# Kernel optimization log

Measured on AMD Instinct MI355X. Metric: run time of the kernel, lower is better.

## Reference

```python
import jax, jax.numpy as jnp
import numpy as np


def setup_inputs() -> dict:
    key = jax.random.key(0)
    ks = jax.random.split(key, 5)
    B, S, I, H, O = 64, 2048, 128, 512, 128
    inputs = jax.random.normal(ks[0], (B, S, I), dtype=jnp.float32)
    h0 = jnp.zeros((B, H), dtype=jnp.float32)
    # Xavier-uniform for W_in / W_out, orthogonal-ish scaled for W_rec
    lim_in = float(np.sqrt(6.0 / (I + H)))
    W_in_w = jax.random.uniform(ks[1], (H, I), minval=-lim_in, maxval=lim_in, dtype=jnp.float32)
    W_in_b = jnp.zeros((H,), dtype=jnp.float32)
    # orthogonal init scaled by 0.9 (matches nn.init.orthogonal_ * 0.9)
    A = jax.random.normal(ks[2], (H, H), dtype=jnp.float32)
    Q, _ = jnp.linalg.qr(A)
    W_rec_w = (0.9 * Q).astype(jnp.float32)
    lim_out = float(np.sqrt(6.0 / (H + O)))
    W_out_w = jax.random.uniform(ks[3], (O, H), minval=-lim_out, maxval=lim_out, dtype=jnp.float32)
    W_out_b = jnp.zeros((O,), dtype=jnp.float32)
    return {
        "inputs": inputs, "h0": h0,
        "W_in_w": W_in_w, "W_in_b": W_in_b,
        "W_rec_w": W_rec_w,
        "W_out_w": W_out_w, "W_out_b": W_out_b,
    }


def reference(inputs, h0, W_in_w, W_in_b, W_rec_w, W_out_w, W_out_b):
    # Precompute the input projection for all timesteps in one big GEMM:
    # (B, S, I) @ (I, H) -> (B, S, H). Faithful: W_in(x_t) = x_t @ W_in_w.T + b.
    xin = jnp.einsum('bsi,hi->bsh', inputs, W_in_w) + W_in_b

    def step(h, x_t):  # x_t: (B, H) pre-projected input at time t
        h_new = jnp.tanh(x_t + h @ W_rec_w.T)  # W_rec has no bias
        return h_new, h_new

    # scan over time axis; move time to leading axis
    h_final, hs = jax.lax.scan(step, h0, jnp.swapaxes(xin, 0, 1))  # hs: (S, B, H)
    hs = jnp.swapaxes(hs, 0, 1)  # (B, S, H)
    outputs = jnp.einsum('bsh,oh->bso', hs, W_out_w) + W_out_b  # (B, S, O)
    return outputs, h_final
```

## Files before the change

### kernel.cpp

```cpp
#include <hip/hip_runtime.h>


typedef _Float16 half2_t __attribute__((ext_vector_type(2)));
typedef _Float16 half8_t __attribute__((ext_vector_type(8)));
typedef float    float2_t __attribute__((ext_vector_type(2)));
typedef float    float4_t __attribute__((ext_vector_type(4)));

#define BB 64
#define SS 2048
#define IN 128
#define HH 512
#define OO 128

using u16 = unsigned short;
using u32 = unsigned int;
using u64 = unsigned long long;

__device__ __forceinline__ float fdot2f(half2_t a, half2_t b, float c) {
#if __has_builtin(__builtin_amdgcn_fdot2)
    return __builtin_amdgcn_fdot2(a, b, c, false);
#else
    return c + (float)a[0] * (float)b[0] + (float)a[1] * (float)b[1];
#endif
}
__device__ __forceinline__ half2_t h2(float a, float b) {
    return half2_t{(_Float16)a, (_Float16)b};
}
__device__ __forceinline__ float fast_tanh(float x) {
    x = fminf(8.0f, fmaxf(-8.0f, x));
#if __has_builtin(__builtin_amdgcn_exp2f) && __has_builtin(__builtin_amdgcn_rcpf)
    const float t = __builtin_amdgcn_exp2f(x * 2.885390081777927f);
    return 1.0f - 2.0f * __builtin_amdgcn_rcpf(t + 1.0f);
#else
    return tanhf(x);
#endif
}
__device__ __forceinline__ void barrier_lds() {
    asm volatile("s_waitcnt lgkmcnt(0)\n\ts_barrier" ::: "memory");
}

__device__ __forceinline__ float red8(float v) {
    int i;
    i = __builtin_amdgcn_update_dpp(0, __builtin_bit_cast(int, v),
                                    0xB1, 0xF, 0xF, true);
    v += __builtin_bit_cast(float, i);
    i = __builtin_amdgcn_update_dpp(0, __builtin_bit_cast(int, v),
                                    0x4E, 0xF, 0xF, true);
    v += __builtin_bit_cast(float, i);
    i = __builtin_amdgcn_update_dpp(0, __builtin_bit_cast(int, v),
                                    0x141, 0xF, 0xF, true);
    v += __builtin_bit_cast(float, i);
    return v;
}
__device__ __forceinline__ float sel8(const float a[8], int c) {
    float v = a[0];
    v = (c == 1) ? a[1] : v;  v = (c == 2) ? a[2] : v;
    v = (c == 3) ? a[3] : v;  v = (c == 4) ? a[4] : v;
    v = (c == 5) ? a[5] : v;  v = (c == 6) ? a[6] : v;
    v = (c == 7) ? a[7] : v;
    return v;
}

__global__ __launch_bounds__(512, 2) void rnn_xin(
    const float* __restrict__ inputs,
    const float* __restrict__ W_in,
    const float* __restrict__ W_in_b,
    u16* __restrict__ xws)
{
    const int tid = threadIdx.x;
    const int c   = tid & 7;
    const int q   = tid >> 3;
    const float bmy = W_in_b[tid];

    half2_t wi8[8][8];
    #pragma unroll
    for (int jj = 0; jj < 8; ++jj) {
        const float4_t* r = (const float4_t*)(W_in + (q * 8 + jj) * IN + c * 16);
        #pragma unroll
        for (int m = 0; m < 4; ++m) {
            const float4_t u = r[m];
            wi8[jj][m * 2 + 0] = h2(u[0], u[1]);
            wi8[jj][m * 2 + 1] = h2(u[2], u[3]);
        }
    }

    const int row0 = blockIdx.x * 512;
    for (int r = 0; r < 512; ++r) {
        const size_t row = row0 + r;
        const float4_t* xr = (const float4_t*)(inputs + row * IN + c * 16);
        half2_t xv[8];
        #pragma unroll
        for (int m = 0; m < 4; ++m) {
            const float4_t u = xr[m];
            xv[m * 2 + 0] = h2(u[0], u[1]);
            xv[m * 2 + 1] = h2(u[2], u[3]);
        }
        float acc[8] = {0, 0, 0, 0, 0, 0, 0, 0};
        #pragma unroll
        for (int jj = 0; jj < 8; ++jj)
            #pragma unroll
            for (int m = 0; m < 8; ++m)
                acc[jj] = fdot2f(wi8[jj][m], xv[m], acc[jj]);
        #pragma unroll
        for (int jj = 0; jj < 8; ++jj) acc[jj] = red8(acc[jj]);
        const float out = sel8(acc, c) + bmy;
        const _Float16 hf = (_Float16)out;
        xws[row * HH + tid] = __builtin_bit_cast(u16, hf);
    }
}

#define REC_STEP(RB, WB, T)                                                  \
    do {                                                                     \
        u16 xn = 0;                                                          \
        if ((T) + 1 < SS) xn = xp[(size_t)((T) + 1) * HH + tid];             \
        float acc[8] = {0, 0, 0, 0, 0, 0, 0, 0};                             \
        const half2_t* hb = &(RB)[c * 36];                                   \
        _Pragma("unroll")                                                    \
        for (int kb = 0; kb < 8; ++kb) {                                     \
            const half8_t hv = *(const half8_t*)(hb + kb * 4);               \
            const half2_t p0 = __builtin_shufflevector(hv, hv, 0, 1);        \
            const half2_t p1 = __builtin_shufflevector(hv, hv, 2, 3);        \
            const half2_t p2 = __builtin_shufflevector(hv, hv, 4, 5);        \
            const half2_t p3 = __builtin_shufflevector(hv, hv, 6, 7);        \
            _Pragma("unroll")                                                \
            for (int jj = 0; jj < 6; ++jj) {                                 \
                acc[jj] = fdot2f(wr[jj][kb * 4 + 0], p0, acc[jj]);           \
                acc[jj] = fdot2f(wr[jj][kb * 4 + 1], p1, acc[jj]);           \
                acc[jj] = fdot2f(wr[jj][kb * 4 + 2], p2, acc[jj]);           \
                acc[jj] = fdot2f(wr[jj][kb * 4 + 3], p3, acc[jj]);           \
            }                                                                \
            const half8_t w6 = *(const half8_t*)(wb6 + (size_t)kb * 2048);   \
            acc[6] = fdot2f(__builtin_shufflevector(w6, w6, 0, 1), p0, acc[6]); \
            acc[6] = fdot2f(__builtin_shufflevector(w6, w6, 2, 3), p1, acc[6]); \
            acc[6] = fdot2f(__builtin_shufflevector(w6, w6, 4, 5), p2, acc[6]); \
            acc[6] = fdot2f(__builtin_shufflevector(w6, w6, 6, 7), p3, acc[6]); \
            const half8_t w7 = *(const half8_t*)(wb7 + (size_t)kb * 2048);   \
            acc[7] = fdot2f(__builtin_shufflevector(w7, w7, 0, 1), p0, acc[7]); \
            acc[7] = fdot2f(__builtin_shufflevector(w7, w7, 2, 3), p1, acc[7]); \
            acc[7] = fdot2f(__builtin_shufflevector(w7, w7, 4, 5), p2, acc[7]); \
            acc[7] = fdot2f(__builtin_shufflevector(w7, w7, 6, 7), p3, acc[7]); \
        }                                                                    \
        _Pragma("unroll")                                                    \
        for (int jj = 0; jj < 8; ++jj) acc[jj] = red8(acc[jj]);              \
        const float hv_new = fast_tanh(sel8(acc, c) + (float)xr);            \
        const _Float16 hf = (_Float16)hv_new;                                \
        xp[(size_t)(T) * HH + tid] = __builtin_bit_cast(u16, hf);            \
        ((_Float16*)(WB))[(tid >> 6) * 72 + (tid & 63)] = hf;                \
        if ((T) == SS - 1) hfinal[bb * HH + tid] = hv_new;                   \
        xr = __builtin_bit_cast(_Float16, xn);                               \
        barrier_lds();                                                       \
    } while (0)

__global__ __launch_bounds__(512, 2) void rnn_rec(
    const float* __restrict__ h0,
    const float* __restrict__ W_rec,
    u16* __restrict__ xws,
    float* __restrict__ hfinal)
{
    const int tid = threadIdx.x;
    const int bb  = blockIdx.x;
    const int c   = tid & 7;
    const int q   = tid >> 3;

    __shared__ __align__(16) half2_t wlin[2 * 8 * 512 * 4];
    __shared__ __align__(16) half2_t hbuf[2][288];

    half2_t wr[6][32];
    #pragma unroll
    for (int jj = 0; jj < 6; ++jj) {
        const float4_t* r = (const float4_t*)(W_rec + (q * 8 + jj) * HH + c * 64);
        #pragma unroll
        for (int m = 0; m < 16; ++m) {
            const float4_t u = r[m];
            wr[jj][m * 2 + 0] = h2(u[0], u[1]);
            wr[jj][m * 2 + 1] = h2(u[2], u[3]);
        }
    }
    #pragma unroll
    for (int jl = 0; jl < 2; ++jl) {
        const int j = q * 8 + 6 + jl;
        #pragma unroll
        for (int kb = 0; kb < 8; ++kb) {
            const float4_t u0 = *(const float4_t*)(W_rec + j * HH + c * 64 + kb * 8);
            const float4_t u1 = *(const float4_t*)(W_rec + j * HH + c * 64 + kb * 8 + 4);
            half8_t pack = half8_t{
                (_Float16)u0[0], (_Float16)u0[1], (_Float16)u0[2], (_Float16)u0[3],
                (_Float16)u1[0], (_Float16)u1[1], (_Float16)u1[2], (_Float16)u1[3]};
            *(half8_t*)&wlin[((jl * 8 + kb) * 512 + tid) * 4] = pack;
        }
    }
    ((_Float16*)hbuf[0])[(tid >> 6) * 72 + (tid & 63)] = (_Float16)h0[bb * HH + tid];

    u16* xp = xws + (size_t)bb * SS * HH;
    _Float16 xr = __builtin_bit_cast(_Float16, xp[tid]);
    __syncthreads();

    const half2_t* wb6 = &wlin[(size_t)tid * 4];
    const half2_t* wb7 = &wlin[(size_t)(8 * 512 + tid) * 4];

    for (int t = 0; t < SS; t += 2) {
        REC_STEP(hbuf[0], hbuf[1], t);
        REC_STEP(hbuf[1], hbuf[0], t + 1);
    }
}

__global__ __launch_bounds__(512, 2) void rnn_out(
    const u16* __restrict__ xws,
    const float* __restrict__ W_out,
    const float* __restrict__ W_out_b,
    float* __restrict__ outp)
{
    const int tid = threadIdx.x;
    const int c   = tid & 7;
    const int wv  = tid >> 6;
    const int lq  = (tid >> 3) & 7;
    const int o0  = wv * 16 + lq * 2;

    half2_t wo2[2][32];
    #pragma unroll
    for (int oo = 0; oo < 2; ++oo) {
        const float4_t* r = (const float4_t*)(W_out + (o0 + oo) * HH + c * 64);
        #pragma unroll
        for (int m = 0; m < 16; ++m) {
            const float4_t u = r[m];
            wo2[oo][m * 2 + 0] = h2(u[0], u[1]);
            wo2[oo][m * 2 + 1] = h2(u[2], u[3]);
        }
    }
    const float b0 = W_out_b[o0], b1 = W_out_b[o0 + 1];

    const int row0 = blockIdx.x * 512;
    for (int r = 0; r < 512; ++r) {
        const size_t row = row0 + r;
        const _Float16* hsrow = (const _Float16*)xws + row * HH + c * 64;
        float a0 = 0.f, a1 = 0.f;
        #pragma unroll
        for (int kb = 0; kb < 8; ++kb) {
            const half8_t hv = *(const half8_t*)(hsrow + kb * 8);
            const half2_t p0 = __builtin_shufflevector(hv, hv, 0, 1);
            const half2_t p1 = __builtin_shufflevector(hv, hv, 2, 3);
            const half2_t p2 = __builtin_shufflevector(hv, hv, 4, 5);
            const half2_t p3 = __builtin_shufflevector(hv, hv, 6, 7);
            a0 = fdot2f(wo2[0][kb * 4 + 0], p0, a0);
            a0 = fdot2f(wo2[0][kb * 4 + 1], p1, a0);
            a0 = fdot2f(wo2[0][kb * 4 + 2], p2, a0);
            a0 = fdot2f(wo2[0][kb * 4 + 3], p3, a0);
            a1 = fdot2f(wo2[1][kb * 4 + 0], p0, a1);
            a1 = fdot2f(wo2[1][kb * 4 + 1], p1, a1);
            a1 = fdot2f(wo2[1][kb * 4 + 2], p2, a1);
            a1 = fdot2f(wo2[1][kb * 4 + 3], p3, a1);
        }
        a0 = red8(a0);
        a1 = red8(a1);
        if (c == 0)
            *(float2_t*)(outp + row * OO + o0) = float2_t{a0 + b0, a1 + b1};
    }
}

__global__ __launch_bounds__(512, 1) void rnn_fused_fb(
    const float* __restrict__ inputs, const float* __restrict__ h0,
    const float* __restrict__ W_in, const float* __restrict__ W_in_b,
    const float* __restrict__ W_rec, const float* __restrict__ W_out,
    const float* __restrict__ W_out_b, float* __restrict__ outp,
    float* __restrict__ hfinal, u64* __restrict__ hex)
{
    const int tid = threadIdx.x;
    const int bb = blockIdx.x >> 1;
    const int w  = blockIdx.x & 1;
    const int c  = tid & 7;
    const int q  = tid >> 3;
    const int og = w * 64 + q;
    const int s  = c >> 2;
    const int oc = w * 4 + (c & 3);
    const int pc = (1 - w) * 4 + (c & 3);
    const int pw = 1 - w;

    __shared__ __align__(16) half2_t hbuf[288];
    __shared__ __align__(16) half2_t xh[2][96];

    half2_t wro[4][16]; half2_t wrp[4][16]; half2_t wi[4][8];
    half2_t woo[16]; half2_t wop[16]; float bias[4];

    #pragma unroll
    for (int jj = 0; jj < 4; ++jj) {
        const int jg = w * 256 + q * 4 + jj;
        const float4_t* ro = (const float4_t*)(W_rec + jg * HH + oc * 64 + s * 32);
        const float4_t* rp = (const float4_t*)(W_rec + jg * HH + pc * 64 + s * 32);
        #pragma unroll
        for (int m = 0; m < 8; ++m) {
            const float4_t uo = ro[m];
            wro[jj][m * 2 + 0] = h2(uo[0], uo[1]);
            wro[jj][m * 2 + 1] = h2(uo[2], uo[3]);
            const float4_t up = rp[m];
            wrp[jj][m * 2 + 0] = h2(up[0], up[1]);
            wrp[jj][m * 2 + 1] = h2(up[2], up[3]);
        }
        const float4_t* irow = (const float4_t*)(W_in + jg * IN + c * 16);
        #pragma unroll
        for (int m = 0; m < 4; ++m) {
            const float4_t u = irow[m];
            wi[jj][m * 2 + 0] = h2(u[0], u[1]);
            wi[jj][m * 2 + 1] = h2(u[2], u[3]);
        }
        bias[jj] = W_in_b[jg];
    }
    {
        const float4_t* oo = (const float4_t*)(W_out + og * HH + oc * 64 + s * 32);
        const float4_t* op = (const float4_t*)(W_out + og * HH + pc * 64 + s * 32);
        #pragma unroll
        for (int m = 0; m < 8; ++m) {
            const float4_t uo = oo[m];
            woo[m * 2 + 0] = h2(uo[0], uo[1]);
            woo[m * 2 + 1] = h2(uo[2], uo[3]);
            const float4_t up = op[m];
            wop[m * 2 + 0] = h2(up[0], up[1]);
            wop[m * 2 + 1] = h2(up[2], up[3]);
        }
    }
    const float bo = W_out_b[og];

    if (tid < 256) {
        const float2_t u = *(const float2_t*)(h0 + bb * HH + tid * 2);
        const int k = tid * 2;
        hbuf[(k >> 6) * 36 + ((k & 63) >> 1)] = h2(u[0], u[1]);
    }
    if (tid >= 256 && tid < 320) {
        const int i2 = tid - 256;
        const float2_t u = *(const float2_t*)(inputs + (size_t)(bb * SS) * IN + i2 * 2);
        xh[0][(i2 >> 3) * 12 + (i2 & 7)] = h2(u[0], u[1]);
    }
    __syncthreads();

    for (int t = 0; t < SS; ++t) {
        const int cur = t & 1;
        float2_t xr;
        const bool xload = (tid >= 256 && tid < 320) && (t + 1 < SS);
        if (xload)
            xr = *(const float2_t*)(inputs + (size_t)(bb * SS + (t + 1)) * IN + (tid - 256) * 2);

        float acc[4] = {0.f, 0.f, 0.f, 0.f};
        float oa = 0.f;
        {
            const half2_t* hb = &hbuf[oc * 36 + s * 16];
            #pragma unroll
            for (int ob = 0; ob < 4; ++ob) {
                const half8_t hv = *(const half8_t*)(hb + ob * 4);
                const half2_t p0 = __builtin_shufflevector(hv, hv, 0, 1);
                const half2_t p1 = __builtin_shufflevector(hv, hv, 2, 3);
                const half2_t p2 = __builtin_shufflevector(hv, hv, 4, 5);
                const half2_t p3 = __builtin_shufflevector(hv, hv, 6, 7);
                #pragma unroll
                for (int jj = 0; jj < 4; ++jj) {
                    acc[jj] = fdot2f(wro[jj][ob * 4 + 0], p0, acc[jj]);
                    acc[jj] = fdot2f(wro[jj][ob * 4 + 1], p1, acc[jj]);
                    acc[jj] = fdot2f(wro[jj][ob * 4 + 2], p2, acc[jj]);
                    acc[jj] = fdot2f(wro[jj][ob * 4 + 3], p3, acc[jj]);
                }
                oa = fdot2f(woo[ob * 4 + 0], p0, oa);
                oa = fdot2f(woo[ob * 4 + 1], p1, oa);
                oa = fdot2f(woo[ob * 4 + 2], p2, oa);
                oa = fdot2f(woo[ob * 4 + 3], p3, oa);
            }
        }
        const int sidx = ((bb * 2 + pw) * 2 + (cur ^ 1)) * 128 + tid;
        u64 spec = 0;
        if (t > 0 && tid < 128)
            spec = __hip_atomic_load(&hex[sidx], __ATOMIC_RELAXED,
                                     __HIP_MEMORY_SCOPE_AGENT);
        {
            const half2_t* xb = &xh[cur][c * 12];
            const half8_t xv0 = *(const half8_t*)(xb);
            const half8_t xv1 = *(const half8_t*)(xb + 4);
            const half2_t x0 = __builtin_shufflevector(xv0, xv0, 0, 1);
            const half2_t x1 = __builtin_shufflevector(xv0, xv0, 2, 3);
            const half2_t x2 = __builtin_shufflevector(xv0, xv0, 4, 5);
            const half2_t x3 = __builtin_shufflevector(xv0, xv0, 6, 7);
            const half2_t x4 = __builtin_shufflevector(xv1, xv1, 0, 1);
            const half2_t x5 = __builtin_shufflevector(xv1, xv1, 2, 3);
            const half2_t x6 = __builtin_shufflevector(xv1, xv1, 4, 5);
            const half2_t x7 = __builtin_shufflevector(xv1, xv1, 6, 7);
            #pragma unroll
            for (int jj = 0; jj < 4; ++jj) {
                acc[jj] = fdot2f(wi[jj][0], x0, acc[jj]);
                acc[jj] = fdot2f(wi[jj][1], x1, acc[jj]);
                acc[jj] = fdot2f(wi[jj][2], x2, acc[jj]);
                acc[jj] = fdot2f(wi[jj][3], x3, acc[jj]);
                acc[jj] = fdot2f(wi[jj][4], x4, acc[jj]);
                acc[jj] = fdot2f(wi[jj][5], x5, acc[jj]);
                acc[jj] = fdot2f(wi[jj][6], x6, acc[jj]);
                acc[jj] = fdot2f(wi[jj][7], x7, acc[jj]);
            }
        }
        if (t > 0 && tid < 128) {
            u64 v = spec;
            if ((u32)(v >> 32) != (u32)t) {
                do {
                    v = __hip_atomic_load(&hex[sidx], __ATOMIC_RELAXED,
                                          __HIP_MEMORY_SCOPE_AGENT);
                } while ((u32)(v >> 32) != (u32)t);
            }
            const int kg = pw * 256 + tid * 2;
            hbuf[(kg >> 6) * 36 + ((kg & 63) >> 1)] =
                __builtin_bit_cast(half2_t, (u32)v);
        }
        barrier_lds();
        {
            const half2_t* hb = &hbuf[pc * 36 + s * 16];
            #pragma unroll
            for (int ob = 0; ob < 4; ++ob) {
                const half8_t hv = *(const half8_t*)(hb + ob * 4);
                const half2_t p0 = __builtin_shufflevector(hv, hv, 0, 1);
                const half2_t p1 = __builtin_shufflevector(hv, hv, 2, 3);
                const half2_t p2 = __builtin_shufflevector(hv, hv, 4, 5);
                const half2_t p3 = __builtin_shufflevector(hv, hv, 6, 7);
                #pragma unroll
                for (int jj = 0; jj < 4; ++jj) {
                    acc[jj] = fdot2f(wrp[jj][ob * 4 + 0], p0, acc[jj]);
                    acc[jj] = fdot2f(wrp[jj][ob * 4 + 1], p1, acc[jj]);
                    acc[jj] = fdot2f(wrp[jj][ob * 4 + 2], p2, acc[jj]);
                    acc[jj] = fdot2f(wrp[jj][ob * 4 + 3], p3, acc[jj]);
                }
                oa = fdot2f(wop[ob * 4 + 0], p0, oa);
                oa = fdot2f(wop[ob * 4 + 1], p1, oa);
                oa = fdot2f(wop[ob * 4 + 2], p2, oa);
                oa = fdot2f(wop[ob * 4 + 3], p3, oa);
            }
        }
        #pragma unroll
        for (int jj = 0; jj < 4; ++jj) {
            float v = acc[jj];
            v += __shfl_xor(v, 1);
            v += __shfl_xor(v, 2);
            v += __shfl_xor(v, 4);
            acc[jj] = v;
        }
        oa += __shfl_xor(oa, 1);
        oa += __shfl_xor(oa, 2);
        oa += __shfl_xor(oa, 4);
        {
            const bool hi = (c & 1) != 0;
            const float a0 = hi ? acc[2] : acc[0];
            const float a1 = hi ? acc[3] : acc[1];
            const float b0 = hi ? bias[2] : bias[0];
            const float b1 = hi ? bias[3] : bias[1];
            const float va = fast_tanh(a0 + b0);
            const float vb = fast_tanh(a1 + b1);
            if (c < 2) {
                const half2_t hx = h2(va, vb);
                const u64 pay = (((u64)(u32)(t + 1)) << 32) |
                                (u64)__builtin_bit_cast(u32, hx);
                const int slot = ((bb * 2 + w) * 2 + cur) * 128 + q * 2 + c;
                __hip_atomic_store(&hex[slot], pay, __ATOMIC_RELAXED,
                                   __HIP_MEMORY_SCOPE_AGENT);
                const int kg = w * 256 + q * 4 + c * 2;
                hbuf[(kg >> 6) * 36 + ((kg & 63) >> 1)] = hx;
                if (t == SS - 1)
                    *(float2_t*)(&hfinal[bb * HH + w * 256 + q * 4 + c * 2]) =
                        float2_t{va, vb};
            }
            if (c == 2 && t > 0)
                outp[(size_t)(bb * SS + (t - 1)) * OO + og] = oa + bo;
        }
        if (xload) {
            const int i2 = tid - 256;
            xh[cur ^ 1][(i2 >> 3) * 12 + (i2 & 7)] = h2(xr[0], xr[1]);
        }
        barrier_lds();
    }

    if (tid < 128) {
        const int sidx = ((bb * 2 + pw) * 2 + ((SS - 1) & 1)) * 128 + tid;
        u64 v;
        do {
            v = __hip_atomic_load(&hex[sidx], __ATOMIC_RELAXED,
                                  __HIP_MEMORY_SCOPE_AGENT);
        } while ((u32)(v >> 32) != (u32)SS);
        const int kg = pw * 256 + tid * 2;
        hbuf[(kg >> 6) * 36 + ((kg & 63) >> 1)] =
            __builtin_bit_cast(half2_t, (u32)v);
    }
    __syncthreads();
    {
        float oa = 0.f;
        const half2_t* ho = &hbuf[oc * 36 + s * 16];
        const half2_t* hp = &hbuf[pc * 36 + s * 16];
        #pragma unroll
        for (int ob = 0; ob < 4; ++ob) {
            const half8_t hv = *(const half8_t*)(ho + ob * 4);
            oa = fdot2f(woo[ob * 4 + 0], __builtin_shufflevector(hv, hv, 0, 1), oa);
            oa = fdot2f(woo[ob * 4 + 1], __builtin_shufflevector(hv, hv, 2, 3), oa);
            oa = fdot2f(woo[ob * 4 + 2], __builtin_shufflevector(hv, hv, 4, 5), oa);
            oa = fdot2f(woo[ob * 4 + 3], __builtin_shufflevector(hv, hv, 6, 7), oa);
        }
        #pragma unroll
        for (int ob = 0; ob < 4; ++ob) {
            const half8_t hv = *(const half8_t*)(hp + ob * 4);
            oa = fdot2f(wop[ob * 4 + 0], __builtin_shufflevector(hv, hv, 0, 1), oa);
            oa = fdot2f(wop[ob * 4 + 1], __builtin_shufflevector(hv, hv, 2, 3), oa);
            oa = fdot2f(wop[ob * 4 + 2], __builtin_shufflevector(hv, hv, 4, 5), oa);
            oa = fdot2f(wop[ob * 4 + 3], __builtin_shufflevector(hv, hv, 6, 7), oa);
        }
        oa += __shfl_xor(oa, 1);
        oa += __shfl_xor(oa, 2);
        oa += __shfl_xor(oa, 4);
        if (c == 0)
            outp[(size_t)(bb * SS + (SS - 1)) * OO + og] = oa + bo;
    }
}

extern "C" void kernel_launch(void* const* d_in, const int* in_sizes, int n_in,
                              void* d_out, int out_size, void* d_ws, size_t ws_size,
                              hipStream_t stream) {
    const float* inputs  = (const float*)d_in[0];
    const float* h0      = (const float*)d_in[1];
    const float* W_in_w  = (const float*)d_in[2];
    const float* W_in_b  = (const float*)d_in[3];
    const float* W_rec_w = (const float*)d_in[4];
    const float* W_out_w = (const float*)d_in[5];
    const float* W_out_b = (const float*)d_in[6];

    float* out    = (float*)d_out;
    float* hfinal = out + (size_t)BB * SS * OO;

    const size_t xin_bytes = (size_t)BB * SS * HH * sizeof(u16);
    if (ws_size >= xin_bytes) {
        u16* xws = (u16*)d_ws;
        rnn_xin<<<dim3(256), dim3(512), 0, stream>>>(inputs, W_in_w, W_in_b, xws);
        rnn_rec<<<dim3(BB), dim3(512), 0, stream>>>(h0, W_rec_w, xws, hfinal);
        rnn_out<<<dim3(256), dim3(512), 0, stream>>>(xws, W_out_w, W_out_b, out);
    } else {
        u64* hex = (u64*)d_ws;
        rnn_fused_fb<<<dim3(BB * 2), dim3(512), 0, stream>>>(
            inputs, h0, W_in_w, W_in_b, W_rec_w, W_out_w, W_out_b,
            out, hfinal, hex);
    }
}
```

Measured before the change: 4.462 ms.

## Keep seven recurrent weight rows in registers, double-buffer input loads, split GEMM grids

```diff
diff --git a/kernel.cpp b/kernel.cpp
--- a/kernel.cpp
+++ b/kernel.cpp
@@ -61,6 +61,32 @@
     return v;
 }
 
+#define XLOAD(B, R)                                                          \
+    do {                                                                     \
+        const float4_t* xr_ = (const float4_t*)(inputs + (size_t)(R) * IN + c * 16); \
+        (B)[0] = xr_[0]; (B)[1] = xr_[1]; (B)[2] = xr_[2]; (B)[3] = xr_[3];  \
+    } while (0)
+#define XCOMP(B, R)                                                          \
+    do {                                                                     \
+        half2_t xv[8];                                                       \
+        _Pragma("unroll")                                                    \
+        for (int m = 0; m < 4; ++m) {                                        \
+            xv[m * 2 + 0] = h2((B)[m][0], (B)[m][1]);                        \
+            xv[m * 2 + 1] = h2((B)[m][2], (B)[m][3]);                        \
+        }                                                                    \
+        float acc[8] = {0, 0, 0, 0, 0, 0, 0, 0};                             \
+        _Pragma("unroll")                                                    \
+        for (int jj = 0; jj < 8; ++jj)                                       \
+            _Pragma("unroll")                                                \
+            for (int m = 0; m < 8; ++m)                                      \
+                acc[jj] = fdot2f(wi8[jj][m], xv[m], acc[jj]);                \
+        _Pragma("unroll")                                                    \
+        for (int jj = 0; jj < 8; ++jj) acc[jj] = red8(acc[jj]);              \
+        const float out_ = sel8(acc, c) + bmy;                               \
+        const _Float16 hf_ = (_Float16)out_;                                 \
+        xws[(size_t)(R) * HH + tid] = __builtin_bit_cast(u16, hf_);          \
+    } while (0)
+
 __global__ __launch_bounds__(512, 2) void rnn_xin(
     const float* __restrict__ inputs,
     const float* __restrict__ W_in,
@@ -84,28 +110,14 @@
         }
     }
 
-    const int row0 = blockIdx.x * 512;
-    for (int r = 0; r < 512; ++r) {
-        const size_t row = row0 + r;
-        const float4_t* xr = (const float4_t*)(inputs + row * IN + c * 16);
-        half2_t xv[8];
-        #pragma unroll
-        for (int m = 0; m < 4; ++m) {
-            const float4_t u = xr[m];
-            xv[m * 2 + 0] = h2(u[0], u[1]);
-            xv[m * 2 + 1] = h2(u[2], u[3]);
-        }
-        float acc[8] = {0, 0, 0, 0, 0, 0, 0, 0};
-        #pragma unroll
-        for (int jj = 0; jj < 8; ++jj)
-            #pragma unroll
-            for (int m = 0; m < 8; ++m)
-                acc[jj] = fdot2f(wi8[jj][m], xv[m], acc[jj]);
-        #pragma unroll
-        for (int jj = 0; jj < 8; ++jj) acc[jj] = red8(acc[jj]);
-        const float out = sel8(acc, c) + bmy;
-        const _Float16 hf = (_Float16)out;
-        xws[row * HH + tid] = __builtin_bit_cast(u16, hf);
+    const int row0 = blockIdx.x * 256;
+    float4_t bA[4], bB[4];
+    XLOAD(bA, row0);
+    for (int r = 0; r < 256; r += 2) {
+        XLOAD(bB, row0 + r + 1);
+        XCOMP(bA, row0 + r);
+        if (r + 2 < 256) XLOAD(bA, row0 + r + 2);
+        XCOMP(bB, row0 + r + 1);
     }
 }
 
@@ -123,18 +135,13 @@
             const half2_t p2 = __builtin_shufflevector(hv, hv, 4, 5);        \
             const half2_t p3 = __builtin_shufflevector(hv, hv, 6, 7);        \
             _Pragma("unroll")                                                \
-            for (int jj = 0; jj < 6; ++jj) {                                 \
+            for (int jj = 0; jj < 7; ++jj) {                                 \
                 acc[jj] = fdot2f(wr[jj][kb * 4 + 0], p0, acc[jj]);           \
                 acc[jj] = fdot2f(wr[jj][kb * 4 + 1], p1, acc[jj]);           \
                 acc[jj] = fdot2f(wr[jj][kb * 4 + 2], p2, acc[jj]);           \
                 acc[jj] = fdot2f(wr[jj][kb * 4 + 3], p3, acc[jj]);           \
             }                                                                \
-            const half8_t w6 = *(const half8_t*)(wb6 + (size_t)kb * 2048);   \
-            acc[6] = fdot2f(__builtin_shufflevector(w6, w6, 0, 1), p0, acc[6]); \
-            acc[6] = fdot2f(__builtin_shufflevector(w6, w6, 2, 3), p1, acc[6]); \
-            acc[6] = fdot2f(__builtin_shufflevector(w6, w6, 4, 5), p2, acc[6]); \
-            acc[6] = fdot2f(__builtin_shufflevector(w6, w6, 6, 7), p3, acc[6]); \
-            const half8_t w7 = *(const half8_t*)(wb7 + (size_t)kb * 2048);   \
+            const half8_t w7 = *(const half8_t*)(wb7 + kb * 2048);           \
             acc[7] = fdot2f(__builtin_shufflevector(w7, w7, 0, 1), p0, acc[7]); \
             acc[7] = fdot2f(__builtin_shufflevector(w7, w7, 2, 3), p1, acc[7]); \
             acc[7] = fdot2f(__builtin_shufflevector(w7, w7, 4, 5), p2, acc[7]); \
@@ -151,7 +158,8 @@
         barrier_lds();                                                       \
     } while (0)
 
-__global__ __launch_bounds__(512, 2) void rnn_rec(
+__global__ __attribute__((amdgpu_waves_per_eu(2, 2)))
+__launch_bounds__(512) void rnn_rec(
     const float* __restrict__ h0,
     const float* __restrict__ W_rec,
     u16* __restrict__ xws,
@@ -162,12 +170,12 @@
     const int c   = tid & 7;
     const int q   = tid >> 3;
 
-    __shared__ __align__(16) half2_t wlin[2 * 8 * 512 * 4];
+    __shared__ __align__(16) half2_t wlin[8 * 512 * 4];
     __shared__ __align__(16) half2_t hbuf[2][288];
 
-    half2_t wr[6][32];
+    half2_t wr[7][32];
     #pragma unroll
-    for (int jj = 0; jj < 6; ++jj) {
+    for (int jj = 0; jj < 7; ++jj) {
         const float4_t* r = (const float4_t*)(W_rec + (q * 8 + jj) * HH + c * 64);
         #pragma unroll
         for (int m = 0; m < 16; ++m) {
@@ -176,9 +184,8 @@
             wr[jj][m * 2 + 1] = h2(u[2], u[3]);
         }
     }
-    #pragma unroll
-    for (int jl = 0; jl < 2; ++jl) {
-        const int j = q * 8 + 6 + jl;
+    {
+        const int j = q * 8 + 7;
         #pragma unroll
         for (int kb = 0; kb < 8; ++kb) {
             const float4_t u0 = *(const float4_t*)(W_rec + j * HH + c * 64 + kb * 8);
@@ -186,7 +193,7 @@
             half8_t pack = half8_t{
                 (_Float16)u0[0], (_Float16)u0[1], (_Float16)u0[2], (_Float16)u0[3],
                 (_Float16)u1[0], (_Float16)u1[1], (_Float16)u1[2], (_Float16)u1[3]};
-            *(half8_t*)&wlin[((jl * 8 + kb) * 512 + tid) * 4] = pack;
+            *(half8_t*)&wlin[(kb * 512 + tid) * 4] = pack;
         }
     }
     ((_Float16*)hbuf[0])[(tid >> 6) * 72 + (tid & 63)] = (_Float16)h0[bb * HH + tid];
@@ -195,8 +202,7 @@
     _Float16 xr = __builtin_bit_cast(_Float16, xp[tid]);
     __syncthreads();
 
-    const half2_t* wb6 = &wlin[(size_t)tid * 4];
-    const half2_t* wb7 = &wlin[(size_t)(8 * 512 + tid) * 4];
+    const half2_t* wb7 = &wlin[tid * 4];
 
     for (int t = 0; t < SS; t += 2) {
         REC_STEP(hbuf[0], hbuf[1], t);
@@ -229,8 +235,8 @@
     }
     const float b0 = W_out_b[o0], b1 = W_out_b[o0 + 1];
 
-    const int row0 = blockIdx.x * 512;
-    for (int r = 0; r < 512; ++r) {
+    const int row0 = blockIdx.x * 256;
+    for (int r = 0; r < 256; ++r) {
         const size_t row = row0 + r;
         const _Float16* hsrow = (const _Float16*)xws + row * HH + c * 64;
         float a0 = 0.f, a1 = 0.f;
@@ -525,9 +531,9 @@
     const size_t xin_bytes = (size_t)BB * SS * HH * sizeof(u16);
     if (ws_size >= xin_bytes) {
         u16* xws = (u16*)d_ws;
-        rnn_xin<<<dim3(256), dim3(512), 0, stream>>>(inputs, W_in_w, W_in_b, xws);
+        rnn_xin<<<dim3(512), dim3(512), 0, stream>>>(inputs, W_in_w, W_in_b, xws);
         rnn_rec<<<dim3(BB), dim3(512), 0, stream>>>(h0, W_rec_w, xws, hfinal);
-        rnn_out<<<dim3(256), dim3(512), 0, stream>>>(xws, W_out_w, W_out_b, out);
+        rnn_out<<<dim3(512), dim3(512), 0, stream>>>(xws, W_out_w, W_out_b, out);
     } else {
         u64* hex = (u64*)d_ws;
         rnn_fused_fb<<<dim3(BB * 2), dim3(512), 0, stream>>>(
```

Result: faster. 4.295 ms (-3.7%).
